# Kernel tuning notes

Measured on AMD Instinct MI355X. Metric: run time of the kernel, lower is better.

Reference implementation:

```python
import jax, jax.numpy as jnp
import numpy as np


def setup_inputs() -> dict:
    key = jax.random.key(0)
    k1, k2, k3 = jax.random.split(key, 3)
    B, T, F = 16, 2048, 64
    he = jax.random.normal(k1, (B, T, F), dtype=jnp.float32)
    scale = 1.0 / np.sqrt(F).astype(np.float32)
    W1 = jax.random.normal(k2, (F, F), dtype=jnp.float32) * scale
    W2 = jax.random.normal(k3, (F, F), dtype=jnp.float32) * scale
    return {"he": he, "W1": W1, "W2": W2, "attention_len": 48}


def reference(he, W1, W2, attention_len):
    # he: [B, T, F] encoder states. For each output step i the original module:
    #   1) unrolls L_i = min(attention_len, max(i,1)) decoder steps starting
    #      from he[:, i, :]:  H_k = sigmoid(H_{k-1} @ W1), Y_k = sigmoid(H_k @ W2)
    #   2) attends Y_1..Y_{L_i} against the encoder window he[:, i-L_i:i, :]
    #      with per-step dot-product scores, softmax over the window, and a
    #      weighted sum of the encoder window.
    # (i=0 degenerates to a single-element softmax -> context = he[:, 0, :].)
    B, T, F = he.shape
    A = attention_len

    def step(H, _):
        H = jax.nn.sigmoid(H @ W1)          # [B, T, F]
        Y = jax.nn.sigmoid(H @ W2)          # [B, T, F]
        return H, Y

    # Decoder outputs for every start position, all A steps: Ys[b, i, t, f]
    _, Ys = jax.lax.scan(step, he, None, length=A)   # [A, B, T, F]
    Ys = jnp.moveaxis(Ys, 0, 2)                      # [B, T, A, F]

    i = jnp.arange(T)[:, None]                       # [T, 1]
    t = jnp.arange(A)[None, :]                       # [1, A]
    L = jnp.minimum(A, jnp.maximum(i, 1))            # window length per step
    j = jnp.clip(i - L + t, 0, T - 1)                # encoder index per (i, t)
    valid = t < L                                    # [T, A]

    gathered = he[:, j, :]                           # [B, T, A, F] windowed encoder
    scores = jnp.einsum('btaf,btaf->bta', Ys, gathered)
    scores = jnp.where(valid[None, :, :], scores, jnp.float32(-1e9))
    w = jax.nn.softmax(scores, axis=-1)              # [B, T, A]
    ctx = jnp.einsum('bta,btaf->btf', w, gathered)   # [B, T, F]
    return ctx
```

## Files before the change

kernel.cpp:

```cpp
#include <hip/hip_runtime.h>

#define B_   16
#define T_   2048
#define F_   64
#define A_   48
#define TOK  64
#define WSTR 68
#define HWS  72
#define SSTR 49
#define NWIN 111

typedef __attribute__((ext_vector_type(4))) _Float16 half4;
typedef __attribute__((ext_vector_type(2))) _Float16 half2;
typedef __attribute__((ext_vector_type(4))) float    f32x4;

#define LOG2E 1.4426950408889634f

__device__ __forceinline__ float sigp(float c) {
    return __builtin_amdgcn_rcpf(1.0f + __builtin_amdgcn_exp2f(c));
}
__device__ __forceinline__ half2 pk2(float a, float b) {
    return __builtin_bit_cast(half2, __builtin_amdgcn_cvt_pkrtz(a, b));
}

struct Smem {
    float    sWin[NWIN * WSTR];
    _Float16 sWinH[NWIN * HWS];
    float    sSc[TOK * SSTR];
};

template<bool FIRST>
__device__ __forceinline__ void run_block(Smem& sm, int b, int t0,
                                          const float* __restrict__ he,
                                          const float* __restrict__ W1,
                                          const float* __restrict__ W2,
                                          float* __restrict__ out)
{
    const int tid = threadIdx.x;
    const float* __restrict__ heB = he + (size_t)b * T_ * F_;

    for (int i = tid; i < NWIN * 16; i += 256) {
        int row = i >> 4, c4 = (i & 15) * 4;
        int g = t0 - 48 + row;
        if (!FIRST || g >= 0) {
            float4 v = *(const float4*)(heB + (size_t)g * F_ + c4);
            *(float4*)(&sm.sWin[row * WSTR + c4]) = v;
            half2 lo = pk2(v.x, v.y), hi = pk2(v.z, v.w);
            half4 h; h[0] = lo[0]; h[1] = lo[1]; h[2] = hi[0]; h[3] = hi[1];
            *(half4*)(&sm.sWinH[row * HWS + c4]) = h;
        }
    }

    const int lane = tid & 63;
    const int wv   = tid >> 6;
    const int quad = lane >> 4;
    const int ml   = lane & 15;
    const int tw0  = wv * 16;
    const int tg   = t0 + tw0 + ml;
    const int L    = min(A_, max(tg, 1));

    half4 aW1[4][4], aW2[4][4];
    for (int mo = 0; mo < 4; ++mo)
        for (int kt = 0; kt < 4; ++kt) {
            half4 f1, f2;
#pragma unroll
            for (int j = 0; j < 4; ++j) {
                int k = kt * 16 + quad * 4 + j;
                f1[j] = (_Float16)(-LOG2E * W1[k * F_ + mo * 16 + ml]);
                f2[j] = (_Float16)(-LOG2E * W2[k * F_ + mo * 16 + ml]);
            }
            aW1[mo][kt] = f1; aW2[mo][kt] = f2;
        }

    half4 hb[4];
#pragma unroll
    for (int kt = 0; kt < 4; ++kt) {
        float4 v = *(const float4*)(heB + (size_t)tg * F_ + kt * 16 + quad * 4);
        half4 h;
        h[0] = (_Float16)v.x; h[1] = (_Float16)v.y;
        h[2] = (_Float16)v.z; h[3] = (_Float16)v.w;
        hb[kt] = h;
    }
    __syncthreads();

    const bool amDiag = (quad == (ml >> 2));
    const bool s0 = (ml & 3) == 0, s1 = (ml & 3) == 1, s2 = (ml & 3) == 2;
    float* scp = &sm.sSc[(tw0 + ml) * SSTR];

    const _Float16* wrow = &sm.sWinH[(tw0 + ml) * HWS + quad * 4];

#pragma unroll 4
    for (int a = 0; a < A_; ++a) {
        f32x4 c1[4];
#pragma unroll
        for (int mo = 0; mo < 4; ++mo) {
            f32x4 z = {0.f, 0.f, 0.f, 0.f};
#pragma unroll
            for (int kt = 0; kt < 4; ++kt)
                z = __builtin_amdgcn_mfma_f32_16x16x16f16(aW1[mo][kt], hb[kt], z, 0, 0, 0);
            c1[mo] = z;
        }
#pragma unroll
        for (int mo = 0; mo < 4; ++mo) {
            half2 lo = pk2(sigp(c1[mo][0]), sigp(c1[mo][1]));
            half2 hi = pk2(sigp(c1[mo][2]), sigp(c1[mo][3]));
            half4 h; h[0] = lo[0]; h[1] = lo[1]; h[2] = hi[0]; h[3] = hi[1];
            hb[mo] = h;
        }
        f32x4 c2[4];
#pragma unroll
        for (int mo = 0; mo < 4; ++mo) {
            f32x4 z = {0.f, 0.f, 0.f, 0.f};
#pragma unroll
            for (int kt = 0; kt < 4; ++kt)
                z = __builtin_amdgcn_mfma_f32_16x16x16f16(aW2[mo][kt], hb[kt], z, 0, 0, 0);
            c2[mo] = z;
        }
        half4 yh[4];
#pragma unroll
        for (int mo = 0; mo < 4; ++mo) {
            half2 lo = pk2(sigp(c2[mo][0]), sigp(c2[mo][1]));
            half2 hi = pk2(sigp(c2[mo][2]), sigp(c2[mo][3]));
            half4 h; h[0] = lo[0]; h[1] = lo[1]; h[2] = hi[0]; h[3] = hi[1];
            yh[mo] = h;
        }
        const _Float16* wp;
        if (FIRST) {
            int j = tg - L + a; if (j < 0) j = 0;
            wp = &sm.sWinH[(j + 48) * HWS + quad * 4];
        } else {
            wp = wrow; wrow += HWS;
        }
        half4 g0 = *(const half4*)(wp);
        half4 g1 = *(const half4*)(wp + 16);
        half4 g2 = *(const half4*)(wp + 32);
        half4 g3 = *(const half4*)(wp + 48);
        f32x4 zs = {0.f, 0.f, 0.f, 0.f};
        zs = __builtin_amdgcn_mfma_f32_16x16x16f16(yh[0], g0, zs, 0, 0, 0);
        zs = __builtin_amdgcn_mfma_f32_16x16x16f16(yh[1], g1, zs, 0, 0, 0);
        zs = __builtin_amdgcn_mfma_f32_16x16x16f16(yh[2], g2, zs, 0, 0, 0);
        zs = __builtin_amdgcn_mfma_f32_16x16x16f16(yh[3], g3, zs, 0, 0, 0);
        float val = s0 ? zs[0] : (s1 ? zs[1] : (s2 ? zs[2] : zs[3]));
        if (FIRST) val = (a < L) ? val : -1e9f;
        if (amDiag) scp[a] = val;
    }
    __syncthreads();

    {
        int r = tid >> 2, s = tid & 3;
        float sc[12];
#pragma unroll
        for (int i = 0; i < 12; ++i) sc[i] = sm.sSc[r * SSTR + i * 4 + s];
        float m = sc[0];
#pragma unroll
        for (int i = 1; i < 12; ++i) m = fmaxf(m, sc[i]);
        m = fmaxf(m, __shfl_xor(m, 1));
        m = fmaxf(m, __shfl_xor(m, 2));
        float e[12]; float sum = 0.f;
#pragma unroll
        for (int i = 0; i < 12; ++i) { e[i] = __expf(sc[i] - m); sum += e[i]; }
        sum += __shfl_xor(sum, 1);
        sum += __shfl_xor(sum, 2);
        float inv = __builtin_amdgcn_rcpf(sum);
#pragma unroll
        for (int i = 0; i < 12; ++i) sm.sSc[r * SSTR + i * 4 + s] = e[i] * inv;
    }
    __syncthreads();

    {
        int r = tid >> 2, fc = (tid & 3) * 16;
        int tgr = t0 + r;
        int Lr = min(A_, max(tgr, 1));
        float acc[16];
#pragma unroll
        for (int q = 0; q < 16; ++q) acc[q] = 0.f;
        for (int a = 0; a < A_; ++a) {
            float wgt = sm.sSc[r * SSTR + a];
            int j = tgr - Lr + a;
            if (FIRST) { if (j < 0) j = 0; }
            const float* wp = &sm.sWin[(j - t0 + 48) * WSTR + fc];
#pragma unroll
            for (int q = 0; q < 4; ++q) {
                float4 g = *(const float4*)(wp + q * 4);
                acc[q*4+0] += wgt * g.x; acc[q*4+1] += wgt * g.y;
                acc[q*4+2] += wgt * g.z; acc[q*4+3] += wgt * g.w;
            }
        }
        float* op = out + ((size_t)b * T_ + tgr) * F_ + fc;
#pragma unroll
        for (int q = 0; q < 4; ++q)
            *(float4*)(op + q * 4) = make_float4(acc[q*4], acc[q*4+1], acc[q*4+2], acc[q*4+3]);
    }
}

__global__ __launch_bounds__(256)
void ContextBlock_kernel(const float* __restrict__ he, const float* __restrict__ W1,
                         const float* __restrict__ W2, float* __restrict__ out)
{
    __shared__ Smem sm;
    const int blk = blockIdx.x;
    if (blk < B_ * 31) {
        int b  = blk / 31;
        int t0 = ((blk % 31) + 1) * TOK;
        run_block<false>(sm, b, t0, he, W1, W2, out);
    } else {
        int b = blk - B_ * 31;
        run_block<true>(sm, b, 0, he, W1, W2, out);
    }
}

extern "C" void kernel_launch(void* const* d_in, const int* in_sizes, int n_in,
                              void* d_out, int out_size, void* d_ws, size_t ws_size,
                              hipStream_t stream) {
    const float* he = (const float*)d_in[0];
    const float* W1 = (const float*)d_in[1];
    const float* W2 = (const float*)d_in[2];
    float* out = (float*)d_out;
    hipLaunchKernelGGL(ContextBlock_kernel, dim3(512), dim3(256), 0, stream, he, W1, W2, out);
}
```

Baseline: 124.8 us.

## Split each 16-token recurrence across two waves with LDS exchange, smaller blocks

Each block now handles 16 tokens with 2 waves, and each wave computes half of the 64 output features of the recurrent matmuls. Per step the waves swap their sigmoid halves through double-buffered LDS behind a barrier. The W1 matmul for the next step is issued alongside the W2 matmul to shorten the serial dependency chain. The window is stored only as fp16, and the weighted sum reads fp16 instead of fp32. The grid grows to 2048 blocks to raise parallelism and shorten per-wave serial latency, at the cost of one block-wide barrier per step, reloading the window across overlapping blocks, and lower precision in the context sum.

```diff
diff --git a/kernel.cpp b/kernel.cpp
--- a/kernel.cpp
+++ b/kernel.cpp
@@ -4,29 +4,34 @@
 #define T_   2048
 #define F_   64
 #define A_   48
-#define TOK  64
-#define WSTR 68
+#define TOKB 16
+#define NW   63
 #define HWS  72
-#define SSTR 49
-#define NWIN 111
+#define PSTR 49
+#define LOG2E 1.4426950408889634f
 
 typedef __attribute__((ext_vector_type(4))) _Float16 half4;
-typedef __attribute__((ext_vector_type(2))) _Float16 half2;
+typedef __attribute__((ext_vector_type(8))) _Float16 half8;
+typedef __attribute__((ext_vector_type(2))) _Float16 h2;
 typedef __attribute__((ext_vector_type(4))) float    f32x4;
-
-#define LOG2E 1.4426950408889634f
 
 __device__ __forceinline__ float sigp(float c) {
     return __builtin_amdgcn_rcpf(1.0f + __builtin_amdgcn_exp2f(c));
 }
-__device__ __forceinline__ half2 pk2(float a, float b) {
-    return __builtin_bit_cast(half2, __builtin_amdgcn_cvt_pkrtz(a, b));
+__device__ __forceinline__ h2 pk2(float a, float b) {
+    return __builtin_bit_cast(h2, __builtin_amdgcn_cvt_pkrtz(a, b));
+}
+__device__ __forceinline__ half4 sigpack(f32x4 c) {
+    h2 lo = pk2(sigp(c[0]), sigp(c[1]));
+    h2 hi = pk2(sigp(c[2]), sigp(c[3]));
+    half4 h; h[0] = lo[0]; h[1] = lo[1]; h[2] = hi[0]; h[3] = hi[1];
+    return h;
 }
 
 struct Smem {
-    float    sWin[NWIN * WSTR];
-    _Float16 sWinH[NWIN * HWS];
-    float    sSc[TOK * SSTR];
+    alignas(16) _Float16 sWinH[NW * HWS];
+    alignas(16) float    sPart[2][TOKB * PSTR];
+    alignas(16) _Float16 sXch[2 * 2 * 64 * 8];
 };
 
 template<bool FIRST>
@@ -39,14 +44,13 @@
     const int tid = threadIdx.x;
     const float* __restrict__ heB = he + (size_t)b * T_ * F_;
 
-    for (int i = tid; i < NWIN * 16; i += 256) {
+    for (int i = tid; i < NW * 16; i += 128) {
         int row = i >> 4, c4 = (i & 15) * 4;
         int g = t0 - 48 + row;
         if (!FIRST || g >= 0) {
             float4 v = *(const float4*)(heB + (size_t)g * F_ + c4);
-            *(float4*)(&sm.sWin[row * WSTR + c4]) = v;
-            half2 lo = pk2(v.x, v.y), hi = pk2(v.z, v.w);
-            half4 h; h[0] = lo[0]; h[1] = lo[1]; h[2] = hi[0]; h[3] = hi[1];
+            half4 h; h[0] = (_Float16)v.x; h[1] = (_Float16)v.y;
+                     h[2] = (_Float16)v.z; h[3] = (_Float16)v.w;
             *(half4*)(&sm.sWinH[row * HWS + c4]) = h;
         }
     }
@@ -55,12 +59,12 @@
     const int wv   = tid >> 6;
     const int quad = lane >> 4;
     const int ml   = lane & 15;
-    const int tw0  = wv * 16;
-    const int tg   = t0 + tw0 + ml;
+    const int tg   = t0 + ml;
     const int L    = min(A_, max(tg, 1));
 
-    half4 aW1[4][4], aW2[4][4];
-    for (int mo = 0; mo < 4; ++mo)
+    half4 aW1[2][4], aW2[2][4];
+    for (int m = 0; m < 2; ++m) {
+        int mo = wv * 2 + m;
         for (int kt = 0; kt < 4; ++kt) {
             half4 f1, f2;
 #pragma unroll
@@ -69,144 +73,157 @@
                 f1[j] = (_Float16)(-LOG2E * W1[k * F_ + mo * 16 + ml]);
                 f2[j] = (_Float16)(-LOG2E * W2[k * F_ + mo * 16 + ml]);
             }
-            aW1[mo][kt] = f1; aW2[mo][kt] = f2;
-        }
+            aW1[m][kt] = f1; aW2[m][kt] = f2;
+        }
+    }
 
     half4 hb[4];
 #pragma unroll
     for (int kt = 0; kt < 4; ++kt) {
         float4 v = *(const float4*)(heB + (size_t)tg * F_ + kt * 16 + quad * 4);
-        half4 h;
-        h[0] = (_Float16)v.x; h[1] = (_Float16)v.y;
-        h[2] = (_Float16)v.z; h[3] = (_Float16)v.w;
+        half4 h; h[0] = (_Float16)v.x; h[1] = (_Float16)v.y;
+                 h[2] = (_Float16)v.z; h[3] = (_Float16)v.w;
         hb[kt] = h;
     }
+
+    f32x4 c1[2];
+#pragma unroll
+    for (int m = 0; m < 2; ++m) {
+        f32x4 z = {0.f, 0.f, 0.f, 0.f};
+#pragma unroll
+        for (int kt = 0; kt < 4; ++kt)
+            z = __builtin_amdgcn_mfma_f32_16x16x16f16(aW1[m][kt], hb[kt], z, 0, 0, 0);
+        c1[m] = z;
+    }
+
     __syncthreads();
 
     const bool amDiag = (quad == (ml >> 2));
-    const bool s0 = (ml & 3) == 0, s1 = (ml & 3) == 1, s2 = (ml & 3) == 2;
-    float* scp = &sm.sSc[(tw0 + ml) * SSTR];
-
-    const _Float16* wrow = &sm.sWinH[(tw0 + ml) * HWS + quad * 4];
-
-#pragma unroll 4
+    const bool e0 = (ml & 3) == 0, e1 = (ml & 3) == 1, e2 = (ml & 3) == 2;
+    float* pPart = &sm.sPart[wv][ml * PSTR];
+
+    _Float16* xW0 = &sm.sXch[(0 * 2 + wv) * 512 + lane * 8];
+    _Float16* xW1 = &sm.sXch[(1 * 2 + wv) * 512 + lane * 8];
+    const _Float16* xR0 = &sm.sXch[(0 * 2 + (1 - wv)) * 512 + lane * 8];
+    const _Float16* xR1 = &sm.sXch[(1 * 2 + (1 - wv)) * 512 + lane * 8];
+
+    const _Float16* __restrict__ wrow = &sm.sWinH[ml * HWS + wv * 32 + quad * 4];
+
+#pragma unroll 2
     for (int a = 0; a < A_; ++a) {
-        f32x4 c1[4];
-#pragma unroll
-        for (int mo = 0; mo < 4; ++mo) {
+        const int p = a & 1;
+        half4 h0 = sigpack(c1[0]);
+        half4 h1 = sigpack(c1[1]);
+        half8 w8 = {h0[0],h0[1],h0[2],h0[3], h1[0],h1[1],h1[2],h1[3]};
+        *(half8*)(p ? xW1 : xW0) = w8;
+        __syncthreads();
+        half8 r8 = *(const half8*)(p ? xR1 : xR0);
+        half4 q0 = {r8[0], r8[1], r8[2], r8[3]};
+        half4 q1 = {r8[4], r8[5], r8[6], r8[7]};
+        if (wv == 0) { hb[0] = h0; hb[1] = h1; hb[2] = q0; hb[3] = q1; }
+        else         { hb[0] = q0; hb[1] = q1; hb[2] = h0; hb[3] = h1; }
+
+        const _Float16* gp;
+        if (FIRST) {
+            int j = tg - L + a;
+            if (j < 0) j = 0;
+            if (j > t0 + 14) j = t0 + 14;
+            gp = &sm.sWinH[(j + 48 - t0) * HWS + wv * 32 + quad * 4];
+        } else gp = wrow + a * HWS;
+        half4 gLo = *(const half4*)gp;
+        half4 gHi = *(const half4*)(gp + 16);
+
+        f32x4 c2[2];
+#pragma unroll
+        for (int m = 0; m < 2; ++m) {
             f32x4 z = {0.f, 0.f, 0.f, 0.f};
 #pragma unroll
             for (int kt = 0; kt < 4; ++kt)
-                z = __builtin_amdgcn_mfma_f32_16x16x16f16(aW1[mo][kt], hb[kt], z, 0, 0, 0);
-            c1[mo] = z;
-        }
-#pragma unroll
-        for (int mo = 0; mo < 4; ++mo) {
-            half2 lo = pk2(sigp(c1[mo][0]), sigp(c1[mo][1]));
-            half2 hi = pk2(sigp(c1[mo][2]), sigp(c1[mo][3]));
-            half4 h; h[0] = lo[0]; h[1] = lo[1]; h[2] = hi[0]; h[3] = hi[1];
-            hb[mo] = h;
-        }
-        f32x4 c2[4];
-#pragma unroll
-        for (int mo = 0; mo < 4; ++mo) {
+                z = __builtin_amdgcn_mfma_f32_16x16x16f16(aW2[m][kt], hb[kt], z, 0, 0, 0);
+            c2[m] = z;
+        }
+#pragma unroll
+        for (int m = 0; m < 2; ++m) {
             f32x4 z = {0.f, 0.f, 0.f, 0.f};
 #pragma unroll
             for (int kt = 0; kt < 4; ++kt)
-                z = __builtin_amdgcn_mfma_f32_16x16x16f16(aW2[mo][kt], hb[kt], z, 0, 0, 0);
-            c2[mo] = z;
-        }
-        half4 yh[4];
-#pragma unroll
-        for (int mo = 0; mo < 4; ++mo) {
-            half2 lo = pk2(sigp(c2[mo][0]), sigp(c2[mo][1]));
-            half2 hi = pk2(sigp(c2[mo][2]), sigp(c2[mo][3]));
-            half4 h; h[0] = lo[0]; h[1] = lo[1]; h[2] = hi[0]; h[3] = hi[1];
-            yh[mo] = h;
-        }
-        const _Float16* wp;
-        if (FIRST) {
-            int j = tg - L + a; if (j < 0) j = 0;
-            wp = &sm.sWinH[(j + 48) * HWS + quad * 4];
-        } else {
-            wp = wrow; wrow += HWS;
-        }
-        half4 g0 = *(const half4*)(wp);
-        half4 g1 = *(const half4*)(wp + 16);
-        half4 g2 = *(const half4*)(wp + 32);
-        half4 g3 = *(const half4*)(wp + 48);
+                z = __builtin_amdgcn_mfma_f32_16x16x16f16(aW1[m][kt], hb[kt], z, 0, 0, 0);
+            c1[m] = z;
+        }
+
+        half4 y0 = sigpack(c2[0]);
+        half4 y1 = sigpack(c2[1]);
         f32x4 zs = {0.f, 0.f, 0.f, 0.f};
-        zs = __builtin_amdgcn_mfma_f32_16x16x16f16(yh[0], g0, zs, 0, 0, 0);
-        zs = __builtin_amdgcn_mfma_f32_16x16x16f16(yh[1], g1, zs, 0, 0, 0);
-        zs = __builtin_amdgcn_mfma_f32_16x16x16f16(yh[2], g2, zs, 0, 0, 0);
-        zs = __builtin_amdgcn_mfma_f32_16x16x16f16(yh[3], g3, zs, 0, 0, 0);
-        float val = s0 ? zs[0] : (s1 ? zs[1] : (s2 ? zs[2] : zs[3]));
-        if (FIRST) val = (a < L) ? val : -1e9f;
-        if (amDiag) scp[a] = val;
+        zs = __builtin_amdgcn_mfma_f32_16x16x16f16(y0, gLo, zs, 0, 0, 0);
+        zs = __builtin_amdgcn_mfma_f32_16x16x16f16(y1, gHi, zs, 0, 0, 0);
+        float val = e0 ? zs[0] : (e1 ? zs[1] : (e2 ? zs[2] : zs[3]));
+        if (amDiag) pPart[a] = val;
     }
     __syncthreads();
 
     {
-        int r = tid >> 2, s = tid & 3;
-        float sc[12];
-#pragma unroll
-        for (int i = 0; i < 12; ++i) sc[i] = sm.sSc[r * SSTR + i * 4 + s];
+        int r = tid >> 3, s = tid & 7;
+        int Lr = min(A_, max(t0 + r, 1));
+        float sc[6];
+#pragma unroll
+        for (int i = 0; i < 6; ++i) {
+            int a = i * 8 + s;
+            float v = sm.sPart[0][r * PSTR + a] + sm.sPart[1][r * PSTR + a];
+            if (FIRST) v = (a < Lr) ? v : -1e9f;
+            sc[i] = v;
+        }
         float m = sc[0];
 #pragma unroll
-        for (int i = 1; i < 12; ++i) m = fmaxf(m, sc[i]);
+        for (int i = 1; i < 6; ++i) m = fmaxf(m, sc[i]);
         m = fmaxf(m, __shfl_xor(m, 1));
         m = fmaxf(m, __shfl_xor(m, 2));
-        float e[12]; float sum = 0.f;
-#pragma unroll
-        for (int i = 0; i < 12; ++i) { e[i] = __expf(sc[i] - m); sum += e[i]; }
+        m = fmaxf(m, __shfl_xor(m, 4));
+        float e[6]; float sum = 0.f;
+#pragma unroll
+        for (int i = 0; i < 6; ++i) { e[i] = __expf(sc[i] - m); sum += e[i]; }
         sum += __shfl_xor(sum, 1);
         sum += __shfl_xor(sum, 2);
+        sum += __shfl_xor(sum, 4);
         float inv = __builtin_amdgcn_rcpf(sum);
 #pragma unroll
-        for (int i = 0; i < 12; ++i) sm.sSc[r * SSTR + i * 4 + s] = e[i] * inv;
+        for (int i = 0; i < 6; ++i) sm.sPart[0][r * PSTR + i * 8 + s] = e[i] * inv;
     }
     __syncthreads();
 
     {
-        int r = tid >> 2, fc = (tid & 3) * 16;
+        int r = tid >> 3, fc = (tid & 7) * 8;
         int tgr = t0 + r;
         int Lr = min(A_, max(tgr, 1));
-        float acc[16];
-#pragma unroll
-        for (int q = 0; q < 16; ++q) acc[q] = 0.f;
+        float acc[8];
+#pragma unroll
+        for (int q = 0; q < 8; ++q) acc[q] = 0.f;
         for (int a = 0; a < A_; ++a) {
-            float wgt = sm.sSc[r * SSTR + a];
+            float wgt = sm.sPart[0][r * PSTR + a];
             int j = tgr - Lr + a;
-            if (FIRST) { if (j < 0) j = 0; }
-            const float* wp = &sm.sWin[(j - t0 + 48) * WSTR + fc];
-#pragma unroll
-            for (int q = 0; q < 4; ++q) {
-                float4 g = *(const float4*)(wp + q * 4);
-                acc[q*4+0] += wgt * g.x; acc[q*4+1] += wgt * g.y;
-                acc[q*4+2] += wgt * g.z; acc[q*4+3] += wgt * g.w;
+            if (FIRST) {
+                if (j < 0) j = 0;
+                if (j > t0 + 14) j = t0 + 14;
             }
+            half8 g = *(const half8*)(&sm.sWinH[(j - t0 + 48) * HWS + fc]);
+#pragma unroll
+            for (int q = 0; q < 8; ++q) acc[q] += wgt * (float)g[q];
         }
         float* op = out + ((size_t)b * T_ + tgr) * F_ + fc;
-#pragma unroll
-        for (int q = 0; q < 4; ++q)
-            *(float4*)(op + q * 4) = make_float4(acc[q*4], acc[q*4+1], acc[q*4+2], acc[q*4+3]);
-    }
-}
-
-__global__ __launch_bounds__(256)
+        *(float4*)(op)     = make_float4(acc[0], acc[1], acc[2], acc[3]);
+        *(float4*)(op + 4) = make_float4(acc[4], acc[5], acc[6], acc[7]);
+    }
+}
+
+__global__ __launch_bounds__(128, 4)
 void ContextBlock_kernel(const float* __restrict__ he, const float* __restrict__ W1,
                          const float* __restrict__ W2, float* __restrict__ out)
 {
     __shared__ Smem sm;
     const int blk = blockIdx.x;
-    if (blk < B_ * 31) {
-        int b  = blk / 31;
-        int t0 = ((blk % 31) + 1) * TOK;
-        run_block<false>(sm, b, t0, he, W1, W2, out);
-    } else {
-        int b = blk - B_ * 31;
-        run_block<true>(sm, b, 0, he, W1, W2, out);
-    }
+    const int b  = blk >> 7;
+    const int t0 = (blk & 127) << 4;
+    if (t0 >= 48) run_block<false>(sm, b, t0, he, W1, W2, out);
+    else          run_block<true >(sm, b, t0, he, W1, W2, out);
 }
 
 extern "C" void kernel_launch(void* const* d_in, const int* in_sizes, int n_in,
@@ -216,5 +233,5 @@
     const float* W1 = (const float*)d_in[1];
     const float* W2 = (const float*)d_in[2];
     float* out = (float*)d_out;
-    hipLaunchKernelGGL(ContextBlock_kernel, dim3(512), dim3(256), 0, stream, he, W1, W2, out);
-}
+    hipLaunchKernelGGL(ContextBlock_kernel, dim3(2048), dim3(128), 0, stream, he, W1, W2, out);
+}
```

Result: slower. 129.0 us (+3.4%).
